# Optimization experiments

Hardware: AMD Instinct MI355X
Metric: run time of the kernel (lower is better)

Reference implementation:

```python
import jax, jax.numpy as jnp
import numpy as np


def setup_inputs() -> dict:
    key = jax.random.key(0)
    k1, k2 = jax.random.split(key)
    seq_len, batch, vocab = 2048, 32, 512
    x = jax.random.normal(k1, (seq_len, batch, vocab), dtype=jnp.float32)
    lengths = jax.random.randint(k2, (batch,), 1, seq_len + 1, dtype=jnp.int32)
    return {"x": x, "lengths": lengths, "blank_index": 0}


def reference(x, lengths, blank_index):
    """CTC greedy decode.

    Faithful to the torch module: argmax over vocab, then per-sequence removal
    of blanks and consecutive duplicates, truncated at `lengths`. Since jit
    forbids ragged outputs, we return (tokens, out_lengths) where tokens is
    (batch, seq_len) left-packed and padded with -1; tokens[b, :out_lengths[b]]
    equals the Python List[int] the original module would produce for batch b.
    """
    seq_len, batch, vocab = x.shape
    ml = jnp.argmax(x, axis=2).T.astype(jnp.int32)  # (batch, seq_len)
    idx = jnp.arange(seq_len, dtype=jnp.int32)
    valid = idx[None, :] < lengths[:, None]
    # prev symbol; -1 sentinel at t=0 (never equals a real symbol or blank)
    prev = jnp.concatenate(
        [jnp.full((batch, 1), -1, ml.dtype), ml[:, :-1]], axis=1
    )
    # keep if non-blank AND (prev was blank OR symbol changed). prev==-1 at t=0
    # makes (ml != prev) true, matching the `prev is None` branch.
    keep = valid & (ml != blank_index) & ((prev == blank_index) | (ml != prev))
    # stream-compact kept symbols to the left via cumsum-based scatter
    pos = jnp.cumsum(keep.astype(jnp.int32), axis=1) - 1  # target slot
    out_lengths = jnp.sum(keep, axis=1).astype(jnp.int32)
    pos = jnp.where(keep, pos, seq_len)  # dump non-kept into overflow slot
    tokens = jnp.full((batch, seq_len + 1), -1, ml.dtype)
    tokens = tokens.at[jnp.arange(batch)[:, None], pos].set(
        jnp.where(keep, ml, -1)
    )
    return tokens[:, :seq_len], out_lengths
```

## Files before the change

kernel.cpp:

```cpp
#include <hip/hip_runtime.h>
#include <hip/hip_bf16.h>
#include <float.h>

typedef float f32x4 __attribute__((ext_vector_type(4)));
typedef int i32x4 __attribute__((ext_vector_type(4)));

__global__ __launch_bounds__(256) void ctc_argmax_dense(
    const float* __restrict__ x,
    int* __restrict__ ml,
    const int* __restrict__ lengths,
    int* __restrict__ tokens,
    int seq_len, int batch, int vocab) {
    const int nrows = seq_len * batch;

    const int gtid = blockIdx.x * blockDim.x + threadIdx.x;
    const int gstride = gridDim.x * blockDim.x;
    for (int i = gtid; i < nrows; i += gstride) tokens[i] = -1;

    const int lane = threadIdx.x & 63;
    const int wave = blockIdx.x * (blockDim.x >> 6) + (threadIdx.x >> 6);

    int myLen = (lane < batch) ? lengths[lane] : 0;
    int incl = myLen;
#pragma unroll
    for (int off = 1; off < 64; off <<= 1) {
        int n = __shfl_up(incl, off, 64);
        if (lane >= off) incl += n;
    }
    const int total = __shfl(incl, 63, 64);

    const int k0 = wave * 8;
    if (k0 >= total) return;

    const int g = lane >> 3;
    const int sl = lane & 7;
    const int k = k0 + g;
    const bool act = (k < total);

    int pos = 0;
#pragma unroll
    for (int step = 32; step >= 1; step >>= 1) {
        const int probe = pos + step - 1;
        const int v = __shfl(incl, probe, 64);
        if (v <= k) pos += step;
    }
    const int b = pos;
    const int baseRaw = __shfl(incl, (b == 0) ? 0 : b - 1, 64);
    const int base = (b == 0) ? 0 : baseRaw;
    const int t = k - base;

    float best = -FLT_MAX;
    int bidx = vocab;

    if (act) {
        const int vmain = vocab & ~31;
        const float* p = x + ((size_t)t * batch + b) * vocab + sl * 4;
        for (int base2 = 0; base2 < vmain; base2 += 32) {
            f32x4 v = *reinterpret_cast<const f32x4*>(p + base2);
            const int i0 = base2 + sl * 4;
#pragma unroll
            for (int j = 0; j < 4; ++j) {
                if (v[j] > best) { best = v[j]; bidx = i0 + j; }
            }
        }
        for (int i = vmain + sl; i < vocab; i += 8) {
            float v = x[((size_t)t * batch + b) * vocab + i];
            if (v > best) { best = v; bidx = i; }
        }
    }

#pragma unroll
    for (int m = 1; m <= 4; m <<= 1) {
        float ov = __shfl_xor(best, m, 64);
        int oi = __shfl_xor(bidx, m, 64);
        if (ov > best || (ov == best && oi < bidx)) { best = ov; bidx = oi; }
    }

    if (act && sl == 0) {
        ml[(size_t)b * seq_len + t] = bidx;
    }
}

__global__ __launch_bounds__(256) void ctc_argmax_kernel(
    const float* __restrict__ x,
    int* __restrict__ ml,
    const int* __restrict__ lengths,
    int* __restrict__ tokens,
    int seq_len, int batch, int vocab) {
    const int nrows = seq_len * batch;

    const int gtid = blockIdx.x * blockDim.x + threadIdx.x;
    const int gstride = gridDim.x * blockDim.x;
    for (int i = gtid; i < nrows; i += gstride) tokens[i] = -1;

    const int lane = threadIdx.x & 63;
    const int wave = blockIdx.x * (blockDim.x >> 6) + (threadIdx.x >> 6);
    const int row0 = wave * 8;
    if (row0 >= nrows) return;

    const int g = lane >> 3;
    const int sl = lane & 7;
    const int row = row0 + g;

    bool act = false;
    int t = 0, b = 0;
    if (row < nrows) {
        t = row / batch;
        b = row - t * batch;
        act = (t < lengths[b]);
    }
    if (!__any(act)) return;

    float best = -FLT_MAX;
    int bidx = vocab;

    if (act) {
        const int vmain = vocab & ~31;
        const float* p = x + (size_t)row * vocab + sl * 4;
        for (int base = 0; base < vmain; base += 32) {
            f32x4 v = *reinterpret_cast<const f32x4*>(p + base);
            const int i0 = base + sl * 4;
#pragma unroll
            for (int j = 0; j < 4; ++j) {
                if (v[j] > best) { best = v[j]; bidx = i0 + j; }
            }
        }
        for (int i = vmain + sl; i < vocab; i += 8) {
            float v = x[(size_t)row * vocab + i];
            if (v > best) { best = v; bidx = i; }
        }
    }

#pragma unroll
    for (int m = 1; m <= 4; m <<= 1) {
        float ov = __shfl_xor(best, m, 64);
        int oi = __shfl_xor(bidx, m, 64);
        if (ov > best || (ov == best && oi < bidx)) { best = ov; bidx = oi; }
    }

    if (act && sl == 0) {
        ml[(size_t)b * seq_len + t] = bidx;
    }
}

__global__ __launch_bounds__(512) void ctc_compact_kernel(
    const int* __restrict__ ml,
    const int* __restrict__ lengths,
    const int* __restrict__ blank_ptr,
    int* __restrict__ tokens,
    int* __restrict__ out_lengths,
    int seq_len, int batch) {
    constexpr int MAXPER = 16;
    const int b = blockIdx.x;
    if (b >= batch) return;
    const int blank = *blank_ptr;
    const int len = lengths[b];
    const int* row = ml + (size_t)b * seq_len;
    int* out = tokens + (size_t)b * seq_len;

    const int tid = threadIdx.x;
    const int nthr = blockDim.x;
    const int per = (seq_len + nthr - 1) / nthr;

    const int t0 = tid * per;
    int vals[MAXPER];
    unsigned keep_mask = 0;
    int cnt = 0;

    if (per == 4 && t0 + 4 <= seq_len && (seq_len & 3) == 0) {
        i32x4 v4 = *reinterpret_cast<const i32x4*>(row + t0);
        int prev = (t0 == 0) ? -1 : row[t0 - 1];
#pragma unroll
        for (int j = 0; j < 4; ++j) {
            const int t = t0 + j;
            const int v = v4[j];
            const bool k = (t < len) && (v != blank) &&
                           (prev == blank || v != prev);
            vals[j] = v;
            if (k) { keep_mask |= (1u << j); ++cnt; }
            prev = v;
        }
    } else {
        int prev = (t0 == 0) ? -1 : ((t0 - 1 < seq_len) ? row[t0 - 1] : -1);
        for (int j = 0; j < per && j < MAXPER; ++j) {
            const int t = t0 + j;
            if (t >= seq_len) break;
            const int v = row[t];
            const bool k = (t < len) && (v != blank) &&
                           (prev == blank || v != prev);
            vals[j] = v;
            if (k) { keep_mask |= (1u << j); ++cnt; }
            prev = v;
        }
    }

    __shared__ int warp_sums[8];
    const int lane = tid & 63;
    const int wid = tid >> 6;
    int incl = cnt;
#pragma unroll
    for (int off = 1; off < 64; off <<= 1) {
        int n = __shfl_up(incl, off, 64);
        if (lane >= off) incl += n;
    }
    if (lane == 63) warp_sums[wid] = incl;
    __syncthreads();

    int wbase = 0;
    for (int w = 0; w < wid; ++w) wbase += warp_sums[w];
    int pos = wbase + incl - cnt;

    for (int j = 0; j < per && j < MAXPER; ++j) {
        if (keep_mask & (1u << j)) out[pos++] = vals[j];
    }

    if (tid == 0) {
        int total = 0;
        const int nwaves = nthr >> 6;
        for (int w = 0; w < nwaves; ++w) total += warp_sums[w];
        out_lengths[b] = total;
    }
}

extern "C" void kernel_launch(void* const* d_in, const int* in_sizes, int n_in,
                              void* d_out, int out_size, void* d_ws, size_t ws_size,
                              hipStream_t stream) {
    const float* x = (const float*)d_in[0];
    const int* lengths = (const int*)d_in[1];
    const int* blank_ptr = (const int*)d_in[2];

    const int batch = in_sizes[1];
    const int seq_len = (out_size - batch) / batch;
    const int vocab = in_sizes[0] / (seq_len * batch);

    int* tokens = (int*)d_out;
    int* out_lengths = (int*)d_out + (size_t)batch * seq_len;
    int* ml = (int*)d_ws;

    const int nrows = seq_len * batch;
    const int ntasks = (nrows + 7) / 8;
    const int waves_per_block = 4;
    const int blocks1 = (ntasks + waves_per_block - 1) / waves_per_block;
    if (batch <= 64) {
        ctc_argmax_dense<<<blocks1, waves_per_block * 64, 0, stream>>>(
            x, ml, lengths, tokens, seq_len, batch, vocab);
    } else {
        ctc_argmax_kernel<<<blocks1, waves_per_block * 64, 0, stream>>>(
            x, ml, lengths, tokens, seq_len, batch, vocab);
    }

    ctc_compact_kernel<<<batch, 512, 0, stream>>>(
        ml, lengths, blank_ptr, tokens, out_lengths, seq_len, batch);
}
```

Baseline: 20.31 us.

## Enumerate valid rows in time-major order for contiguous dense argmax reads

The dense argmax kernel previously numbered valid (t,b) rows batch-major: sequence b's rows were consecutive, so neighbouring groups read rows strided by batch*vocab. Now each wave binary-searches for the time step where its rows start, using wave-wide reductions of min(len,probe). It then walks time steps with a ballot over active sequences and assigns each group its (t,b) in time-major order. Neighbouring groups therefore read adjacent rows of x, which should improve DRAM and cache locality. The cost is extra per-wave index work: a log(seq_len) search with a 6-step reduction at each step, plus a loop over time steps.

New measurement: 25.43 us. 25.2% more time.

```diff
diff --git a/kernel.cpp b/kernel.cpp
--- a/kernel.cpp
+++ b/kernel.cpp
@@ -19,42 +19,64 @@
 
     const int lane = threadIdx.x & 63;
     const int wave = blockIdx.x * (blockDim.x >> 6) + (threadIdx.x >> 6);
-
-    int myLen = (lane < batch) ? lengths[lane] : 0;
-    int incl = myLen;
-#pragma unroll
-    for (int off = 1; off < 64; off <<= 1) {
-        int n = __shfl_up(incl, off, 64);
-        if (lane >= off) incl += n;
-    }
-    const int total = __shfl(incl, 63, 64);
-
     const int k0 = wave * 8;
+
+    const int lenL = (lane < batch) ? lengths[lane] : 0;
+
+    int total = lenL;
+#pragma unroll
+    for (int m = 1; m < 64; m <<= 1) total += __shfl_xor(total, m, 64);
     if (k0 >= total) return;
+
+    int t0 = 0;
+    int step = 1;
+    while ((step << 1) <= seq_len) step <<= 1;
+    for (; step; step >>= 1) {
+        const int probe = t0 + step;
+        if (probe <= seq_len) {
+            int s = (lenL < probe) ? lenL : probe;
+#pragma unroll
+            for (int m = 1; m < 64; m <<= 1) s += __shfl_xor(s, m, 64);
+            if (s <= k0) t0 = probe;
+        }
+    }
+    int S_run = (lenL < t0) ? lenL : t0;
+#pragma unroll
+    for (int m = 1; m < 64; m <<= 1) S_run += __shfl_xor(S_run, m, 64);
 
     const int g = lane >> 3;
     const int sl = lane & 7;
     const int k = k0 + g;
     const bool act = (k < total);
 
-    int pos = 0;
-#pragma unroll
-    for (int step = 32; step >= 1; step >>= 1) {
-        const int probe = pos + step - 1;
-        const int v = __shfl(incl, probe, 64);
-        if (v <= k) pos += step;
-    }
-    const int b = pos;
-    const int baseRaw = __shfl(incl, (b == 0) ? 0 : b - 1, 64);
-    const int base = (b == 0) ? 0 : baseRaw;
-    const int t = k - base;
+    int myT = -1, myB = 0;
+    int t_u = t0;
+    while (__any((myT < 0) && act)) {
+        const unsigned long long mask = __ballot(lenL > t_u);
+        const int A = __popcll(mask);
+        if ((myT < 0) && act && (k < S_run + A)) {
+            const int myJ = k - S_run;
+            int p = 0;
+            if (__popcll(mask & 0xFFFFFFFFULL) <= myJ) p = 32;
+#pragma unroll
+            for (int w = 16; w; w >>= 1) {
+                const unsigned long long low = (1ULL << (p + w)) - 1ULL;
+                if (__popcll(mask & low) <= myJ) p += w;
+            }
+            myT = t_u;
+            myB = p;
+        }
+        S_run += A;
+        ++t_u;
+        if (t_u > seq_len) break;
+    }
 
     float best = -FLT_MAX;
     int bidx = vocab;
 
-    if (act) {
+    if (act && myT >= 0) {
         const int vmain = vocab & ~31;
-        const float* p = x + ((size_t)t * batch + b) * vocab + sl * 4;
+        const float* p = x + ((size_t)myT * batch + myB) * vocab + sl * 4;
         for (int base2 = 0; base2 < vmain; base2 += 32) {
             f32x4 v = *reinterpret_cast<const f32x4*>(p + base2);
             const int i0 = base2 + sl * 4;
@@ -64,7 +86,7 @@
             }
         }
         for (int i = vmain + sl; i < vocab; i += 8) {
-            float v = x[((size_t)t * batch + b) * vocab + i];
+            float v = x[((size_t)myT * batch + myB) * vocab + i];
             if (v > best) { best = v; bidx = i; }
         }
     }
@@ -76,8 +98,8 @@
         if (ov > best || (ov == best && oi < bidx)) { best = ov; bidx = oi; }
     }
 
-    if (act && sl == 0) {
-        ml[(size_t)b * seq_len + t] = bidx;
+    if (act && myT >= 0 && sl == 0) {
+        ml[(size_t)myB * seq_len + myT] = bidx;
     }
 }
 
```
